# Optimization experiments

Measured on AMD Instinct MI355X. Metric: run time of the kernel, lower is better.

Reference implementation:

```python
import jax, jax.numpy as jnp
import numpy as np

HID = 128
GRID = 8
PRED_LEN = 25


def _lstm_final(x, w_ih, w_hh, b_ih, b_hh):
    """PyTorch-style LSTM over time axis; returns final (h, c). x: [B, T, F]."""
    B = x.shape[0]
    H = w_hh.shape[1]
    # precompute input contribution for all timesteps: [B, T, 4H]
    gx = jnp.einsum('btf,gf->btg', x, w_ih) + b_ih + b_hh

    def step(carry, g):
        h, c = carry
        gates = g + h @ w_hh.T
        i, f, gg, o = jnp.split(gates, 4, axis=-1)  # torch gate order i,f,g,o
        i = jax.nn.sigmoid(i)
        f = jax.nn.sigmoid(f)
        gg = jnp.tanh(gg)
        o = jax.nn.sigmoid(o)
        c = f * c + i * gg
        h = o * jnp.tanh(c)
        return (h, c), None

    h0 = jnp.zeros((B, H), x.dtype)
    (h, c), _ = jax.lax.scan(step, (h0, h0), jnp.swapaxes(gx, 0, 1))
    return h, c


def _conv2d_same(x, w, b):
    y = jax.lax.conv_general_dilated(x, w, (1, 1), 'SAME',
                                     dimension_numbers=('NCHW', 'OIHW', 'NCHW'))
    return y + b[None, :, None, None]


def setup_inputs() -> dict:
    key = jax.random.key(0)
    ks = jax.random.split(key, 24)
    B, K, T, F = 8192, 8, 20, 7
    H = HID
    s = lambda fan: 1.0 / np.sqrt(fan)
    u = lambda k, shape, fan: jax.random.uniform(k, shape, jnp.float32, -s(fan), s(fan))
    inp = {
        'target': jax.random.normal(ks[0], (B, T, F), jnp.float32),
        'neigh_dyn': jax.random.normal(ks[1], (B, K, T, F), jnp.float32),
        'neigh_spatial': jax.random.normal(ks[2], (B, K, 2), jnp.float32),
        'lane': jax.random.normal(ks[3], (B, T), jnp.float32),
        # encoder LSTM
        'enc_w_ih': u(ks[4], (4 * H, F), H), 'enc_w_hh': u(ks[5], (4 * H, H), H),
        'enc_b_ih': u(ks[6], (4 * H,), H), 'enc_b_hh': u(ks[7], (4 * H,), H),
        # neighbor encoder LSTM
        'nb_w_ih': u(ks[8], (4 * H, F), H), 'nb_w_hh': u(ks[9], (4 * H, H), H),
        'nb_b_ih': u(ks[10], (4 * H,), H), 'nb_b_hh': u(ks[11], (4 * H,), H),
        # social conv stack
        'conv1_w': u(ks[12], (H // 2, H, 3, 3), H * 9), 'conv1_b': u(ks[13], (H // 2,), H * 9),
        'conv2_w': u(ks[14], (H // 4, H // 2, 3, 3), (H // 2) * 9), 'conv2_b': u(ks[15], (H // 4,), (H // 2) * 9),
        # fusion linear (H + H//4 -> H)
        'fus_w': u(ks[16], (H, H + H // 4), H + H // 4), 'fus_b': u(ks[17], (H,), H + H // 4),
        # decoder LSTM (input_dim 2)
        'dec_w_ih': u(ks[18], (4 * H, 2), H), 'dec_w_hh': u(ks[19], (4 * H, H), H),
        'dec_b_ih': u(ks[20], (4 * H,), H), 'dec_b_hh': u(ks[21], (4 * H,), H),
        # output linear (H -> 2)
        'out_w': u(ks[22], (2, H), H), 'out_b': u(ks[23], (2,), H),
    }
    return inp


def reference(target, neigh_dyn, neigh_spatial, lane,
              enc_w_ih, enc_w_hh, enc_b_ih, enc_b_hh,
              nb_w_ih, nb_w_hh, nb_b_ih, nb_b_hh,
              conv1_w, conv1_b, conv2_w, conv2_b,
              fus_w, fus_b,
              dec_w_ih, dec_w_hh, dec_b_ih, dec_b_hh,
              out_w, out_b):
    B = target.shape[0]
    K = neigh_dyn.shape[1]
    H = HID

    # encode target trajectory
    h_target, _ = _lstm_final(target, enc_w_ih, enc_w_hh, enc_b_ih, enc_b_hh)  # [B, H]

    # encode neighbors (shared weights) via flattening B*K
    neigh_flat = neigh_dyn.reshape(B * K, neigh_dyn.shape[2], neigh_dyn.shape[3])
    h_neigh, _ = _lstm_final(neigh_flat, nb_w_ih, nb_w_hh, nb_b_ih, nb_b_hh)
    h_neigh = h_neigh.reshape(B, K, H)

    # social pooling: scatter into [B, H, GRID, GRID]
    center = GRID // 2
    n = min(K, GRID * GRID - 1)
    idx = np.arange(n) + 1
    xs = idx % GRID
    ys = idx // GRID
    grid = jnp.zeros((B, H, GRID, GRID), target.dtype)
    grid = grid.at[:, :, center, center].set(h_target)
    grid = grid.at[:, :, ys, xs].set(jnp.swapaxes(h_neigh[:, :n, :], 1, 2))

    x = jax.nn.relu(_conv2d_same(grid, conv1_w, conv1_b))
    x = jax.nn.relu(_conv2d_same(x, conv2_w, conv2_b))
    pooled = jnp.max(x, axis=(2, 3))  # AdaptiveMaxPool2d(1) -> [B, H//4]

    fused = jnp.tanh(jnp.concatenate([h_target, pooled], axis=-1) @ fus_w.T + fus_b)

    dec_bias = dec_b_ih + dec_b_hh

    def dec_step(carry, _):
        h, c, inp = carry
        gates = inp @ dec_w_ih.T + h @ dec_w_hh.T + dec_bias
        i, f, gg, o = jnp.split(gates, 4, axis=-1)
        i = jax.nn.sigmoid(i)
        f = jax.nn.sigmoid(f)
        gg = jnp.tanh(gg)
        o = jax.nn.sigmoid(o)
        c = f * c + i * gg
        h = o * jnp.tanh(c)
        pred = h @ out_w.T + out_b  # [B, 2]
        return (h, c, pred), pred

    h0 = fused
    c0 = jnp.zeros_like(fused)
    inp0 = jnp.zeros((B, 2), target.dtype)
    _, preds = jax.lax.scan(dec_step, (h0, c0, inp0), None, length=PRED_LEN)
    return jnp.swapaxes(preds, 0, 1)  # [B, pred_len, 2]
```

## Files before the change

### kernel.cpp

```cpp
#include <hip/hip_runtime.h>

typedef _Float16 half8  __attribute__((ext_vector_type(8)));
typedef _Float16 half4v __attribute__((ext_vector_type(4)));
typedef float  floatx4  __attribute__((ext_vector_type(4)));

#define MFMA16(A,B,C) __builtin_amdgcn_mfma_f32_16x16x32_f16((A),(B),(C),0,0,0)

#define L2E  1.4426950408889634f
#define L2E2 2.8853900817779268f

__device__ __forceinline__ float rcpf(float x){ return __builtin_amdgcn_rcpf(x); }
__device__ __forceinline__ float ex2(float x){ return __builtin_amdgcn_exp2f(x); }
__device__ __forceinline__ float tanh_raw(float c){
  return 1.0f - 2.0f*rcpf(1.0f + ex2(L2E2*c));
}
__device__ __forceinline__ half8 ld8(const _Float16* p){
  half4v a = *(const half4v*)p;
  half4v b = *(const half4v*)(p+4);
  return __builtin_shufflevector(a,b,0,1,2,3,4,5,6,7);
}

__device__ __forceinline__ float lstm_cell(float yi, float yf, float yg, float yo,
                                           float& c){
  float A = ex2(-yi), B = ex2(-yf), C = ex2(yg);
  float r1 = rcpf(1.0f + B);
  float r2 = rcpf((1.0f + A)*(1.0f + C));
  float cn = c*r1 + (C - 1.0f)*r2;
  c = cn;
  float F = ex2(-yo), E = ex2(L2E2*cn);
  float r3 = rcpf((1.0f + F)*(1.0f + E));
  return (E - 1.0f)*r3;
}

static __device__ constexpr int DY[27] = {0,0,0,0,0,0,0,0, 1,1,1,1,1,1,1,1, 2,2, 3,3,3,4,4,4,5,5,5};
static __device__ constexpr int DX[27] = {0,1,2,3,4,5,6,7, 0,1,2,3,4,5,6,7, 0,1, 3,4,5,3,4,5,3,4,5};
static __device__ constexpr int PY[9]  = {0,0,0,0,0,0,0,1,4};
static __device__ constexpr int PX[9]  = {1,2,3,4,5,6,7,0,4};
static __device__ constexpr int OY[46] = {0,0,0,0,0,0,0,0, 1,1,1,1,1,1,1,1, 2,2,2,2,2,2,2,2,
                                          3,3,3,3,3,3,3, 4,4,4,4,4, 5,5,5,5,5, 6,6,6,6,6};
static __device__ constexpr int OX[46] = {0,1,2,3,4,5,6,7, 0,1,2,3,4,5,6,7, 0,1,2,3,4,5,6,7,
                                          0,1,2,3,4,5,6, 2,3,4,5,6, 2,3,4,5,6, 2,3,4,5,6};
__device__ constexpr int d1idx(int iy,int ix){
  return (iy<0||iy>7||ix<0||ix>7) ? -1 :
         (iy<=1) ? iy*8+ix :
         (iy==2 && ix<=1) ? 16+ix :
         (iy>=3 && iy<=5 && ix>=3 && ix<=5) ? 18+(iy-3)*3+(ix-3) : -1;
}

__global__ __launch_bounds__(512, 4) void lstm_all(
    const float* __restrict__ target, const float* __restrict__ neigh,
    const float* __restrict__ e_wih, const float* __restrict__ e_whh,
    const float* __restrict__ e_bih, const float* __restrict__ e_bhh,
    const float* __restrict__ n_wih, const float* __restrict__ n_whh,
    const float* __restrict__ n_bih, const float* __restrict__ n_bhh,
    _Float16* __restrict__ h_enc16, _Float16* __restrict__ h_nb16)
{
  __shared__ _Float16 h_lds[2][16][136];
  __shared__ _Float16 xf16[16][168];
  __shared__ __align__(16) _Float16 wihb[8][4][17][8];

  const int tid  = threadIdx.x;
  const int wv   = tid >> 6;
  const int lane = tid & 63;
  const int q    = lane >> 4;
  const int cb   = lane & 15;

  const bool enc = (blockIdx.x < 512);
  const float* x   = enc ? target : neigh;
  const float* wih = enc ? e_wih : n_wih;
  const float* whh = enc ? e_whh : n_whh;
  const float* bih = enc ? e_bih : n_bih;
  const float* bhh = enc ? e_bhh : n_bhh;
  _Float16* hout   = enc ? h_enc16 : h_nb16;
  const long base  = enc ? (long)blockIdx.x*16 : (long)(blockIdx.x-512)*16;

  for (int i = tid; i < 16*168; i += 512){
    int seq = i/168, rem = i%168, t = rem>>3, f = rem&7;
    float v = 0.f;
    if (t < 20) v = (f < 7) ? x[base*140 + seq*140 + t*7 + f] : 1.0f;
    xf16[seq][rem] = (_Float16)v;
  }
  for (int i = tid; i < 2*16*136; i += 512) ((_Float16*)h_lds)[i] = (_Float16)0.f;

  if (q == 0){
    #pragma unroll
    for (int g=0; g<4; ++g){
      const float sc = (g==2) ? L2E2 : L2E;
      const int col = g*128 + wv*16 + cb;
      _Float16* d = &wihb[wv][g][cb][0];
      #pragma unroll
      for (int j=0;j<7;++j) d[j] = (_Float16)(wih[col*7+j]*sc);
      d[7] = (_Float16)((bih[col]+bhh[col])*sc);
    }
  } else if (lane == 16){
    #pragma unroll
    for (int g=0; g<4; ++g){
      _Float16* d = &wihb[wv][g][16][0];
      #pragma unroll
      for (int j=0;j<8;++j) d[j] = (_Float16)0.f;
    }
  }

  half8 bfrag[4][4];
  #pragma unroll
  for (int g=0; g<4; ++g){
    const float sc = (g==2) ? L2E2 : L2E;
    const int col = g*128 + wv*16 + cb;
    #pragma unroll
    for (int kc=0; kc<4; ++kc){
      const float* src = whh + (long)col*128 + kc*32 + q*8;
      half8 f;
      #pragma unroll
      for (int j=0;j<8;++j) f[j] = (_Float16)(src[j]*sc);
      bfrag[g][kc] = f;
    }
  }
  __syncthreads();

  const _Float16* bxp = &wihb[wv][0][(q==0)?cb:16][0];
  const _Float16* a4p = (q==0) ? &xf16[cb][0] : &wihb[wv][0][16][0];
  const int a4step = (q==0) ? 8 : 0;
  half8 a4 = *(const half8*)a4p;
  a4p += a4step;

  float c_reg[4] = {0,0,0,0};
  half4v hv = {0,0,0,0};
  const floatx4 ZERO4 = {0.f,0.f,0.f,0.f};

  for (int t=0; t<20; ++t){
    const _Float16* hrow = &h_lds[t&1][cb][0];

    floatx4 acc[4];
    #pragma unroll
    for (int g=0; g<4; ++g){
      half8 bx = *(const half8*)(bxp + g*136);
      acc[g] = MFMA16(bx, a4, ZERO4);
    }
    #pragma unroll
    for (int kc=0; kc<4; ++kc){
      half8 b = *(const half8*)(hrow + kc*32 + q*8);
      #pragma unroll
      for (int g=0; g<4; ++g)
        acc[g] = MFMA16(bfrag[g][kc], b, acc[g]);
    }
    #pragma unroll
    for (int r=0; r<4; ++r)
      hv[r] = (_Float16)lstm_cell(acc[0][r], acc[1][r], acc[2][r], acc[3][r], c_reg[r]);
    *(half4v*)&h_lds[(t+1)&1][cb][wv*16 + q*4] = hv;
    a4 = *(const half8*)a4p;
    a4p += a4step;
    __syncthreads();
  }

  *(half4v*)&hout[(base + cb)*128 + wv*16 + q*4] = hv;
}

__global__ void prep_kernel(const float* __restrict__ w1, const float* __restrict__ b1,
                            const float* __restrict__ w2, const float* __restrict__ b2,
                            const float* __restrict__ fus_w,
                            _Float16* __restrict__ w1f, _Float16* __restrict__ w2f,
                            _Float16* __restrict__ fus_wf,
                            float* __restrict__ v2bg, float* __restrict__ bgmax)
{
  const int tid = threadIdx.x;
  const int gid = blockIdx.x*256 + tid;
  const int gstride = gridDim.x*256;
  for (int i = gid; i < 9*64*128; i += gstride){
    int s = i>>13, rem = i&8191, c1 = rem>>7, ci = rem&127;
    w1f[s*8448 + c1*132 + ci] = (_Float16)w1[c1*1152 + ci*9 + s];
  }
  for (int i = gid; i < 9*32*64; i += gstride){
    int s = i>>11, rem = i&2047, c2 = rem>>6, ci = rem&63;
    w2f[s*2176 + c2*68 + ci] = (_Float16)w2[c2*576 + ci*9 + s];
  }
  for (int i = gid; i < 128*160; i += gstride){
    int n = i/160, k = i%160;
    fus_wf[n*164 + k] = (_Float16)fus_w[i];
  }
  if (blockIdx.x == 0){
    __shared__ float S[288];
    __shared__ int bgm[32];
    for (int i=tid;i<288;i+=256){
      int c2=i/9, s=i%9;
      float a=0.f;
      for (int ci=0;ci<64;++ci) a += w2[c2*576+ci*9+s]*fmaxf(b1[ci],0.f);
      S[i]=a;
    }
    if (tid<32) bgm[tid]=0;
    __syncthreads();
    for (int i=tid;i<2048;i+=256){
      int cell=i>>5, c2=i&31, y=cell>>3, xx=cell&7;
      float a=b2[c2];
      for (int dy=0;dy<3;++dy){ int iy=y+dy-1; if((unsigned)iy>7u) continue;
        for (int dx=0;dx<3;++dx){ int ix=xx+dx-1; if((unsigned)ix>7u) continue;
          a += S[c2*9+dy*3+dx]; } }
      v2bg[cell*32+c2]=a;
      bool aff = (y<=2) || (y==3 && xx<=6) || (y>=4 && y<=6 && xx>=2 && xx<=6);
      if(!aff) atomicMax(&bgm[c2], __float_as_int(fmaxf(a,0.f)));
    }
    __syncthreads();
    if (tid<32) bgmax[tid]=__int_as_float(bgm[tid]);
  }
}

__global__ __launch_bounds__(256, 1) void social_fuse(
    const _Float16* __restrict__ h_enc, const _Float16* __restrict__ h_nb,
    const _Float16* __restrict__ w1f, const _Float16* __restrict__ w2f,
    const _Float16* __restrict__ fus_wf,
    const float* __restrict__ b1, const float* __restrict__ v2bg,
    const float* __restrict__ bgmax, const float* __restrict__ fus_b,
    float* __restrict__ fused)
{
  __shared__ __align__(16) _Float16 vecs[9*16*132];
  __shared__ __align__(16) _Float16 d1[27*16*68];
  __shared__ __align__(16) _Float16 A16[16*164];
  __shared__ int pooled[512];

  const int tid  = threadIdx.x;
  const int wv   = tid >> 6;
  const int lane = tid & 63;
  const int q    = lane >> 4;
  const int cb   = lane & 15;
  const long base = (long)blockIdx.x * 16;

  for (int i=tid; i<9*16*32; i+=256){
    int p = i>>9, rem = i&511, bb = rem>>5, j = rem&31;
    const _Float16* src = (p<8) ? (h_nb + (((base+bb))*8 + p)*128 + j*4)
                                : (h_enc + (base+bb)*128 + j*4);
    *(unsigned long long*)(vecs + p*2112 + bb*132 + j*4) = *(const unsigned long long*)src;
  }
  for (int i=tid; i<512; i+=256){
    int bb=i>>5, j=i&31;
    *(unsigned long long*)(A16 + bb*164 + j*4) =
        *(const unsigned long long*)(h_enc + (base+bb)*128 + j*4);
  }
  for (int i=tid; i<512; i+=256) pooled[i] = __float_as_int(bgmax[i&31]);
  __syncthreads();

  {
    const int c1lane = wv*16 + cb;
    half8 bf1[9][4];
    #pragma unroll
    for (int s=0;s<9;++s)
      #pragma unroll
      for (int kc=0;kc<4;++kc)
        bf1[s][kc] = ld8(w1f + s*8448 + c1lane*132 + kc*32 + q*8);
    const float b1v = b1[c1lane];
    const float bg  = fmaxf(b1v, 0.f);

    #pragma unroll
    for (int ci=0; ci<27; ++ci){
      const int y = DY[ci], x = DX[ci];
      floatx4 C = {0.f,0.f,0.f,0.f};
      #pragma unroll
      for (int p=0;p<9;++p){
        const int dy = PY[p]-y+1, dx = PX[p]-x+1;
        if (dy>=0 && dy<3 && dx>=0 && dx<3){
          const int s = dy*3+dx;
          const _Float16* ap = vecs + p*2112 + cb*132 + q*8;
          #pragma unroll
          for (int kc=0;kc<4;++kc)
            C = MFMA16(ld8(ap + kc*32), bf1[s][kc], C);
        }
      }
      _Float16* dp = d1 + ci*1088 + c1lane;
      #pragma unroll
      for (int r=0;r<4;++r)
        dp[(q*4+r)*68] = (_Float16)(fmaxf(b1v + C[r], 0.f) - bg);
    }
  }
  __syncthreads();

  {
    half8 bf2[9][2][2];
    #pragma unroll
    for (int s=0;s<9;++s)
      #pragma unroll
      for (int nt=0;nt<2;++nt)
        #pragma unroll
        for (int kc=0;kc<2;++kc)
          bf2[s][nt][kc] = ld8(w2f + s*2176 + (nt*16+cb)*68 + kc*32 + q*8);

    float rm0[4] = {0,0,0,0}, rm1[4] = {0,0,0,0};
    #pragma unroll
    for (int oc=0; oc<46; ++oc){
      if ((oc & 3) != wv) continue;
      const int y = OY[oc], x = OX[oc];
      const int cell = y*8+x;
      float v0 = v2bg[cell*32 + cb];
      float v1 = v2bg[cell*32 + 16 + cb];
      floatx4 C0 = {v0,v0,v0,v0}, C1 = {v1,v1,v1,v1};
      #pragma unroll
      for (int dy=0;dy<3;++dy)
        #pragma unroll
        for (int dx=0;dx<3;++dx){
          const int dc = d1idx(y+dy-1, x+dx-1);
          if (dc < 0) continue;
          const int s = dy*3+dx;
          const _Float16* ap = d1 + dc*1088 + cb*68 + q*8;
          #pragma unroll
          for (int kc=0;kc<2;++kc){
            half8 a = ld8(ap + kc*32);
            C0 = MFMA16(a, bf2[s][0][kc], C0);
            C1 = MFMA16(a, bf2[s][1][kc], C1);
          }
        }
      #pragma unroll
      for (int r=0;r<4;++r){
        rm0[r] = fmaxf(rm0[r], fmaxf(C0[r],0.f));
        rm1[r] = fmaxf(rm1[r], fmaxf(C1[r],0.f));
      }
    }
    #pragma unroll
    for (int r=0;r<4;++r){
      atomicMax(&pooled[(q*4+r)*32 + cb],      __float_as_int(rm0[r]));
      atomicMax(&pooled[(q*4+r)*32 + 16 + cb], __float_as_int(rm1[r]));
    }
  }
  __syncthreads();

  for (int i=tid;i<512;i+=256){
    int bb=i>>5, c2=i&31;
    A16[bb*164 + 128 + c2] = (_Float16)__int_as_float(pooled[i]);
  }
  __syncthreads();

  {
    half8 bfF[2][5];
    #pragma unroll
    for (int nt2=0;nt2<2;++nt2)
      #pragma unroll
      for (int kc=0;kc<5;++kc)
        bfF[nt2][kc] = ld8(fus_wf + ((wv*2+nt2)*16+cb)*164 + kc*32 + q*8);
    const float fb0 = fus_b[(wv*2)*16+cb];
    const float fb1 = fus_b[(wv*2+1)*16+cb];
    floatx4 C0 = {0.f,0.f,0.f,0.f}, C1 = {0.f,0.f,0.f,0.f};
    #pragma unroll
    for (int kc=0;kc<5;++kc){
      half8 a = ld8(A16 + cb*164 + kc*32 + q*8);
      C0 = MFMA16(a, bfF[0][kc], C0);
      C1 = MFMA16(a, bfF[1][kc], C1);
    }
    #pragma unroll
    for (int r=0;r<4;++r){
      const long row = base + q*4 + r;
      fused[row*128 + (wv*2)*16+cb]   = tanh_raw(C0[r]+fb0);
      fused[row*128 + (wv*2+1)*16+cb] = tanh_raw(C1[r]+fb1);
    }
  }
}

__global__ __launch_bounds__(512, 4) void dec_mfma(
    const float* __restrict__ fused,
    const float* __restrict__ w_ih, const float* __restrict__ w_hh,
    const float* __restrict__ b_ih, const float* __restrict__ b_hh,
    const float* __restrict__ out_w, const float* __restrict__ out_b,
    float* __restrict__ out)
{
  __shared__ _Float16 h_lds[2][16][136];
  __shared__ __align__(16) _Float16 wib[8][4][17][8];
  __shared__ float ow_lds[2][128];
  __shared__ float pred_lds[16][2];

  const int tid  = threadIdx.x;
  const int wv   = tid >> 6;
  const int lane = tid & 63;
  const int q    = lane >> 4;
  const int cb   = lane & 15;
  const long base = (long)blockIdx.x * 16;

  for (int i=tid;i<256;i+=512) ow_lds[i>>7][i&127] = out_w[i];
  for (int i=tid;i<2048;i+=512) h_lds[0][i>>7][i&127] = (_Float16)fused[base*128 + i];
  for (int i=tid;i<2048;i+=512) h_lds[1][i>>7][i&127] = (_Float16)0.f;
  if (tid<32) pred_lds[tid>>1][tid&1] = 0.f;

  if (q == 0){
    #pragma unroll
    for (int g=0; g<4; ++g){
      const float sc = (g==2) ? L2E2 : L2E;
      const int col = g*128 + wv*16 + cb;
      _Float16* d = &wib[wv][g][cb][0];
      d[0] = (_Float16)(w_ih[col*2+0]*sc);
      d[1] = (_Float16)(w_ih[col*2+1]*sc);
      d[2] = (_Float16)((b_ih[col]+b_hh[col])*sc);
      #pragma unroll
      for (int j=3;j<8;++j) d[j] = (_Float16)0.f;
    }
  } else if (lane == 16){
    #pragma unroll
    for (int g=0; g<4; ++g){
      _Float16* d = &wib[wv][g][16][0];
      #pragma unroll
      for (int j=0;j<8;++j) d[j] = (_Float16)0.f;
    }
  }

  half8 bfrag[4][4];
  #pragma unroll
  for (int g=0; g<4; ++g){
    const float sc = (g==2) ? L2E2 : L2E;
    const int col = g*128 + wv*16 + cb;
    #pragma unroll
    for (int kc=0; kc<4; ++kc){
      const float* src = w_hh + (long)col*128 + kc*32 + q*8;
      half8 f;
      #pragma unroll
      for (int j=0;j<8;++j) f[j] = (_Float16)(src[j]*sc);
      bfrag[g][kc] = f;
    }
  }
  float ob0 = out_b[0], ob1 = out_b[1];
  __syncthreads();

  const _Float16* wibp = &wib[wv][0][(q==0)?cb:16][0];
  float c_reg[4] = {0,0,0,0};
  half4v hv;
  const floatx4 ZERO4 = {0.f,0.f,0.f,0.f};

  for (int t=0; t<25; ++t){
    const _Float16* hrow = &h_lds[t&1][cb][0];

    half8 pb = {0,0,0,0,0,0,0,0};
    if (q == 0){
      pb[0] = (_Float16)pred_lds[cb][0];
      pb[1] = (_Float16)pred_lds[cb][1];
      pb[2] = (_Float16)1.0f;
    }
    floatx4 acc[4];
    #pragma unroll
    for (int g=0; g<4; ++g){
      half8 w = *(const half8*)(wibp + g*136);
      acc[g] = MFMA16(w, pb, ZERO4);
    }
    #pragma unroll
    for (int kc=0; kc<4; ++kc){
      half8 b = *(const half8*)(hrow + kc*32 + q*8);
      #pragma unroll
      for (int g=0; g<4; ++g)
        acc[g] = MFMA16(bfrag[g][kc], b, acc[g]);
    }
    #pragma unroll
    for (int r=0; r<4; ++r)
      hv[r] = (_Float16)lstm_cell(acc[0][r], acc[1][r], acc[2][r], acc[3][r], c_reg[r]);
    _Float16 (*hw)[136] = h_lds[(t+1)&1];
    *(half4v*)&hw[cb][wv*16 + q*4] = hv;
    __syncthreads();
    {
      int pair = tid>>3, part = tid&7;
      if (pair < 32){
        int m = pair>>1, oc = pair&1;
        const float* owp = ow_lds[oc];
        float v = 0.f;
        #pragma unroll
        for (int k=part*16; k<part*16+16; ++k) v += owp[k]*(float)hw[m][k];
        v += __shfl_down(v, 4, 8);
        v += __shfl_down(v, 2, 8);
        v += __shfl_down(v, 1, 8);
        if (part==0){
          v += (oc ? ob1 : ob0);
          pred_lds[m][oc] = v;
          out[(base+m)*50 + t*2 + oc] = v;
        }
      }
    }
    __syncthreads();
  }
}

extern "C" void kernel_launch(void* const* d_in, const int* in_sizes, int n_in,
                              void* d_out, int out_size, void* d_ws, size_t ws_size,
                              hipStream_t stream)
{
  (void)in_sizes; (void)n_in; (void)out_size; (void)ws_size;
  const float* target   = (const float*)d_in[0];
  const float* neigh    = (const float*)d_in[1];
  const float* enc_w_ih = (const float*)d_in[4];
  const float* enc_w_hh = (const float*)d_in[5];
  const float* enc_b_ih = (const float*)d_in[6];
  const float* enc_b_hh = (const float*)d_in[7];
  const float* nb_w_ih  = (const float*)d_in[8];
  const float* nb_w_hh  = (const float*)d_in[9];
  const float* nb_b_ih  = (const float*)d_in[10];
  const float* nb_b_hh  = (const float*)d_in[11];
  const float* w1       = (const float*)d_in[12];
  const float* b1       = (const float*)d_in[13];
  const float* w2       = (const float*)d_in[14];
  const float* b2       = (const float*)d_in[15];
  const float* fus_w    = (const float*)d_in[16];
  const float* fus_b    = (const float*)d_in[17];
  const float* dec_w_ih = (const float*)d_in[18];
  const float* dec_w_hh = (const float*)d_in[19];
  const float* dec_b_ih = (const float*)d_in[20];
  const float* dec_b_hh = (const float*)d_in[21];
  const float* out_w    = (const float*)d_in[22];
  const float* out_b    = (const float*)d_in[23];

  char* ws = (char*)d_ws;
  _Float16* h_nb16  = (_Float16*)ws;
  _Float16* h_enc16 = (_Float16*)(ws + (16u<<20));
  float*    fusedp  = (float*)(ws + (18u<<20));
  char* aux = ws + (22u<<20);
  _Float16* w1f    = (_Float16*)aux;
  _Float16* w2f    = (_Float16*)(aux + 152064);
  _Float16* fus_wf = (_Float16*)(aux + 152064 + 39168);
  float*    v2bg   = (float*)(aux + 233216);
  float*    bgmaxp = (float*)(aux + 241408);

  prep_kernel<<<64, 256, 0, stream>>>(w1, b1, w2, b2, fus_w, w1f, w2f, fus_wf, v2bg, bgmaxp);
  lstm_all<<<4608, 512, 0, stream>>>(target, neigh,
                                     enc_w_ih, enc_w_hh, enc_b_ih, enc_b_hh,
                                     nb_w_ih, nb_w_hh, nb_b_ih, nb_b_hh,
                                     h_enc16, h_nb16);
  social_fuse<<<512, 256, 0, stream>>>(h_enc16, h_nb16, w1f, w2f, fus_wf,
                                       b1, v2bg, bgmaxp, fus_b, fusedp);
  dec_mfma<<<512, 512, 0, stream>>>(fusedp, dec_w_ih, dec_w_hh, dec_b_ih, dec_b_hh,
                                    out_w, out_b, (float*)d_out);
}
```

Before: 526.9 us.

## Fold decoder output projection into recurrent weights to drop feedback sync

Because the decoder input is the previous prediction (a linear function of h), the kernel folds W_ih·out_w into a precomputed W_hh' and W_ih·out_b into the bias, both built in prep_kernel. A one-time negative correction at t=0 accounts for the zero initial input. This removes the per-step input MFMAs and the extra barrier that waited for predictions before the next step; predictions are now only written out. The risk is extra fp16 rounding of the combined weights, and the prep kernel does a little more work.

```diff
diff --git a/kernel.cpp b/kernel.cpp
--- a/kernel.cpp
+++ b/kernel.cpp
@@ -158,8 +158,12 @@
 __global__ void prep_kernel(const float* __restrict__ w1, const float* __restrict__ b1,
                             const float* __restrict__ w2, const float* __restrict__ b2,
                             const float* __restrict__ fus_w,
+                            const float* __restrict__ dec_wih, const float* __restrict__ dec_whh,
+                            const float* __restrict__ dec_bih, const float* __restrict__ dec_bhh,
+                            const float* __restrict__ out_w, const float* __restrict__ out_b,
                             _Float16* __restrict__ w1f, _Float16* __restrict__ w2f,
                             _Float16* __restrict__ fus_wf,
+                            _Float16* __restrict__ whhp, float* __restrict__ biasp,
                             float* __restrict__ v2bg, float* __restrict__ bgmax)
 {
   const int tid = threadIdx.x;
@@ -176,6 +180,17 @@
   for (int i = gid; i < 128*160; i += gstride){
     int n = i/160, k = i%160;
     fus_wf[n*164 + k] = (_Float16)fus_w[i];
+  }
+  for (int i = gid; i < 512*128; i += gstride){
+    int col = i>>7, k = i&127;
+    float sc = ((col>>7)==2) ? L2E2 : L2E;
+    float v = dec_whh[i] + dec_wih[col*2+0]*out_w[k] + dec_wih[col*2+1]*out_w[128+k];
+    whhp[i] = (_Float16)(v*sc);
+  }
+  for (int i = gid; i < 512; i += gstride){
+    float sc = ((i>>7)==2) ? L2E2 : L2E;
+    biasp[i] = (dec_bih[i] + dec_bhh[i] + dec_wih[i*2+0]*out_b[0]
+                + dec_wih[i*2+1]*out_b[1])*sc;
   }
   if (blockIdx.x == 0){
     __shared__ float S[288];
@@ -352,8 +367,8 @@
 
 __global__ __launch_bounds__(512, 4) void dec_mfma(
     const float* __restrict__ fused,
-    const float* __restrict__ w_ih, const float* __restrict__ w_hh,
-    const float* __restrict__ b_ih, const float* __restrict__ b_hh,
+    const _Float16* __restrict__ whhp, const float* __restrict__ biasp,
+    const float* __restrict__ w_ih,
     const float* __restrict__ out_w, const float* __restrict__ out_b,
     float* __restrict__ out)
 {
@@ -372,7 +387,6 @@
   for (int i=tid;i<256;i+=512) ow_lds[i>>7][i&127] = out_w[i];
   for (int i=tid;i<2048;i+=512) h_lds[0][i>>7][i&127] = (_Float16)fused[base*128 + i];
   for (int i=tid;i<2048;i+=512) h_lds[1][i>>7][i&127] = (_Float16)0.f;
-  if (tid<32) pred_lds[tid>>1][tid&1] = 0.f;
 
   if (q == 0){
     #pragma unroll
@@ -380,11 +394,10 @@
       const float sc = (g==2) ? L2E2 : L2E;
       const int col = g*128 + wv*16 + cb;
       _Float16* d = &wib[wv][g][cb][0];
-      d[0] = (_Float16)(w_ih[col*2+0]*sc);
-      d[1] = (_Float16)(w_ih[col*2+1]*sc);
-      d[2] = (_Float16)((b_ih[col]+b_hh[col])*sc);
-      #pragma unroll
-      for (int j=3;j<8;++j) d[j] = (_Float16)0.f;
+      d[0] = (_Float16)(-w_ih[col*2+0]*sc);
+      d[1] = (_Float16)(-w_ih[col*2+1]*sc);
+      #pragma unroll
+      for (int j=2;j<8;++j) d[j] = (_Float16)0.f;
     }
   } else if (lane == 16){
     #pragma unroll
@@ -396,20 +409,33 @@
   }
 
   half8 bfrag[4][4];
+  float bias_r[4][4];
   #pragma unroll
   for (int g=0; g<4; ++g){
-    const float sc = (g==2) ? L2E2 : L2E;
     const int col = g*128 + wv*16 + cb;
     #pragma unroll
-    for (int kc=0; kc<4; ++kc){
-      const float* src = w_hh + (long)col*128 + kc*32 + q*8;
-      half8 f;
-      #pragma unroll
-      for (int j=0;j<8;++j) f[j] = (_Float16)(src[j]*sc);
-      bfrag[g][kc] = f;
-    }
+    for (int r=0; r<4; ++r) bias_r[g][r] = biasp[g*128 + wv*16 + q*4 + r];
+    #pragma unroll
+    for (int kc=0; kc<4; ++kc)
+      bfrag[g][kc] = ld8(whhp + (long)col*128 + kc*32 + q*8);
   }
   float ob0 = out_b[0], ob1 = out_b[1];
+  __syncthreads();
+
+  {
+    int pair = tid>>3, part = tid&7;
+    if (pair < 32){
+      int m = pair>>1, oc = pair&1;
+      const float* owp = ow_lds[oc];
+      float v = 0.f;
+      #pragma unroll
+      for (int k=part*16; k<part*16+16; ++k) v += owp[k]*(float)h_lds[0][m][k];
+      v += __shfl_down(v, 4, 8);
+      v += __shfl_down(v, 2, 8);
+      v += __shfl_down(v, 1, 8);
+      if (part==0) pred_lds[m][oc] = v + (oc ? ob1 : ob0);
+    }
+  }
   __syncthreads();
 
   const _Float16* wibp = &wib[wv][0][(q==0)?cb:16][0];
@@ -420,17 +446,23 @@
   for (int t=0; t<25; ++t){
     const _Float16* hrow = &h_lds[t&1][cb][0];
 
-    half8 pb = {0,0,0,0,0,0,0,0};
-    if (q == 0){
-      pb[0] = (_Float16)pred_lds[cb][0];
-      pb[1] = (_Float16)pred_lds[cb][1];
-      pb[2] = (_Float16)1.0f;
-    }
     floatx4 acc[4];
     #pragma unroll
-    for (int g=0; g<4; ++g){
-      half8 w = *(const half8*)(wibp + g*136);
-      acc[g] = MFMA16(w, pb, ZERO4);
+    for (int g=0; g<4; ++g)
+      #pragma unroll
+      for (int r=0; r<4; ++r) acc[g][r] = bias_r[g][r];
+
+    if (t == 0){
+      half8 pb = {0,0,0,0,0,0,0,0};
+      if (q == 0){
+        pb[0] = (_Float16)pred_lds[cb][0];
+        pb[1] = (_Float16)pred_lds[cb][1];
+      }
+      #pragma unroll
+      for (int g=0; g<4; ++g){
+        half8 w = *(const half8*)(wibp + g*136);
+        acc[g] = MFMA16(w, pb, acc[g]);
+      }
     }
     #pragma unroll
     for (int kc=0; kc<4; ++kc){
@@ -456,14 +488,10 @@
         v += __shfl_down(v, 4, 8);
         v += __shfl_down(v, 2, 8);
         v += __shfl_down(v, 1, 8);
-        if (part==0){
-          v += (oc ? ob1 : ob0);
-          pred_lds[m][oc] = v;
-          out[(base+m)*50 + t*2 + oc] = v;
-        }
+        if (part==0)
+          out[(base+m)*50 + t*2 + oc] = v + (oc ? ob1 : ob0);
       }
     }
-    __syncthreads();
   }
 }
 
@@ -505,14 +533,19 @@
   _Float16* fus_wf = (_Float16*)(aux + 152064 + 39168);
   float*    v2bg   = (float*)(aux + 233216);
   float*    bgmaxp = (float*)(aux + 241408);
-
-  prep_kernel<<<64, 256, 0, stream>>>(w1, b1, w2, b2, fus_w, w1f, w2f, fus_wf, v2bg, bgmaxp);
+  _Float16* whhp   = (_Float16*)(aux + 241536);
+  float*    biasp  = (float*)(aux + 241536 + 131072);
+
+  prep_kernel<<<64, 256, 0, stream>>>(w1, b1, w2, b2, fus_w,
+                                      dec_w_ih, dec_w_hh, dec_b_ih, dec_b_hh,
+                                      out_w, out_b,
+                                      w1f, w2f, fus_wf, whhp, biasp, v2bg, bgmaxp);
   lstm_all<<<4608, 512, 0, stream>>>(target, neigh,
                                      enc_w_ih, enc_w_hh, enc_b_ih, enc_b_hh,
                                      nb_w_ih, nb_w_hh, nb_b_ih, nb_b_hh,
                                      h_enc16, h_nb16);
   social_fuse<<<512, 256, 0, stream>>>(h_enc16, h_nb16, w1f, w2f, fus_wf,
                                        b1, v2bg, bgmaxp, fus_b, fusedp);
-  dec_mfma<<<512, 512, 0, stream>>>(fusedp, dec_w_ih, dec_w_hh, dec_b_ih, dec_b_hh,
+  dec_mfma<<<512, 512, 0, stream>>>(fusedp, whhp, biasp, dec_w_ih,
                                     out_w, out_b, (float*)d_out);
 }
```

After: 505.5 us. 1.04x faster.
